# Kernel optimization log

Measured on AMD Instinct MI355X. Metric: run time of the kernel, lower is better.

Reference implementation:

```python
import jax, jax.numpy as jnp
import numpy as np
import math

B_SZ, T, D_IN, D_OUT, N = 8, 4096, 256, 256, 512
RMIN, RMAX, MAX_PHASE = 0.99, 1.0, 6.283


def setup_inputs() -> dict:
    key = jax.random.key(0)
    ks = jax.random.split(key, 8)
    u_in = jax.random.normal(ks[0], (B_SZ, T, D_IN), dtype=jnp.float32)
    u1 = jax.random.uniform(ks[1], (N,), dtype=jnp.float32)
    u2 = jax.random.uniform(ks[2], (N,), dtype=jnp.float32)
    # LRU parametrization from 'Resurrecting Linear Recurrences'
    nu_log = jnp.log(-0.5 * jnp.log(u1 * (RMAX + RMIN) * (RMAX - RMIN) + RMIN ** 2))
    theta_log = jnp.log(MAX_PHASE * u2)
    lambda_mod = jnp.exp(-jnp.exp(nu_log))
    gamma_log = jnp.log(jnp.sqrt(1.0 - jnp.square(lambda_mod)))
    B_real = jax.random.normal(ks[3], (N, D_IN), dtype=jnp.float32) / math.sqrt(2 * D_IN)
    B_imag = jax.random.normal(ks[4], (N, D_IN), dtype=jnp.float32) / math.sqrt(2 * D_IN)
    C_real = jax.random.normal(ks[5], (D_OUT, N), dtype=jnp.float32) / math.sqrt(N)
    C_imag = jax.random.normal(ks[6], (D_OUT, N), dtype=jnp.float32) / math.sqrt(N)
    D = jax.random.normal(ks[7], (D_OUT, D_IN), dtype=jnp.float32) / math.sqrt(D_IN)
    return {"u_in": u_in, "nu_log": nu_log, "theta_log": theta_log,
            "gamma_log": gamma_log, "B_real": B_real, "B_imag": B_imag,
            "C_real": C_real, "C_imag": C_imag, "D": D}


def _lru_forward(u_in, nu_log, theta_log, gamma_log, B_real, B_imag, C_real, C_imag, D):
    lambda_mod = jnp.exp(-jnp.exp(nu_log))
    theta = jnp.exp(theta_log)
    lam = (lambda_mod * jnp.cos(theta) + 1j * lambda_mod * jnp.sin(theta)).astype(jnp.complex64)  # [N]
    gammas = jnp.exp(gamma_log)
    Bc = (B_real + 1j * B_imag).astype(jnp.complex64)  # [N, D_in]
    Cc = (C_real + 1j * C_imag).astype(jnp.complex64)  # [D_out, N]
    # driving term: gamma * (u_t @ B^T)  -> [b, t, n]
    Bu = gammas.astype(jnp.complex64) * jnp.einsum('bti,ni->btn', u_in.astype(jnp.complex64), Bc)
    # linear recurrence x_t = lam * x_{t-1} + Bu_t, x_0 prior = 0, via associative scan
    a = jnp.broadcast_to(lam, Bu.shape)

    def combine(e1, e2):
        a1, b1 = e1
        a2, b2 = e2
        return a1 * a2, a2 * b1 + b2

    _, x = jax.lax.associative_scan(combine, (a, Bu), axis=1)  # [b, t, n] complex
    y = 2.0 * jnp.real(jnp.einsum('btn,on->bto', x, Cc)) + jnp.einsum('bti,oi->bto', u_in, D)
    return y


def reference(u_in, nu_log, theta_log, gamma_log, B_real, B_imag, C_real, C_imag, D):
    return _lru_forward(u_in, nu_log, theta_log, gamma_log, B_real, B_imag, C_real, C_imag, D)
```

## Files before the change

### kernel.cpp

```cpp
#include <hip/hip_runtime.h>
#include <hip/hip_bf16.h>
#include <math.h>

#define B_SZ    8
#define T_LEN   4096
#define DIN     256
#define DOUT    256
#define NST     512
#define M_ROWS  (B_SZ * T_LEN)
#define N1      (2 * NST)
#define K2      (N1 + DIN)
#define CHL     128
#define NCH     (T_LEN / CHL)

typedef __attribute__((ext_vector_type(8))) short bf16x8;
typedef __attribute__((ext_vector_type(4))) float f32x4;
typedef __hip_bfloat16 bf16;

#define OFF_UBF  67108864
#define OFF_WP   83886080
#define OFF_W2   84410368
#define OFF_LAM  85065728
#define OFF_LAML 85069824
#define OFF_SSUM 85073920

__device__ __forceinline__ void gl_lds16(const bf16* g, bf16* l) {
    __builtin_amdgcn_global_load_lds(
        (const __attribute__((address_space(1))) void*)g,
        (__attribute__((address_space(3))) void*)l, 16, 0, 0);
}

__global__ __launch_bounds__(256) void prep(const float* __restrict__ u,
        const float* __restrict__ nu_log, const float* __restrict__ theta_log,
        const float* __restrict__ gamma_log,
        const float* __restrict__ B_real, const float* __restrict__ B_imag,
        const float* __restrict__ C_real, const float* __restrict__ C_imag,
        const float* __restrict__ Dm,
        bf16* __restrict__ ub, bf16* __restrict__ Wp, bf16* __restrict__ W2,
        float* __restrict__ lam, float* __restrict__ lamL) {
    int bid = blockIdx.x, tid = threadIdx.x;
    if (bid < 8192) {
        int i = bid * 256 + tid;
        float4 v = ((const float4*)u)[i];
        union { bf16 h[4]; uint2 u2; } p;
        p.h[0] = __float2bfloat16(v.x); p.h[1] = __float2bfloat16(v.y);
        p.h[2] = __float2bfloat16(v.z); p.h[3] = __float2bfloat16(v.w);
        ((uint2*)ub)[i] = p.u2;
    } else if (bid < 9216) {
        int c = bid - 8192;
        int n = c & (NST - 1);
        float g = expf(gamma_log[n]);
        const float* src = (c < NST) ? (B_real + (size_t)n * DIN)
                                     : (B_imag + (size_t)n * DIN);
        Wp[(size_t)c * DIN + tid] = __float2bfloat16(g * src[tid]);
        int idx = c * 256 + tid;
        if (idx < NST) {
            float lm = expf(-expf(nu_log[idx]));
            float th = expf(theta_log[idx]);
            float lr = lm * cosf(th), li = lm * sinf(th);
            lam[idx] = lr; lam[NST + idx] = li;
            float ar = lr, ai = li;
#pragma unroll
            for (int q = 0; q < 7; ++q) {
                float nr = ar * ar - ai * ai;
                float ni = 2.f * ar * ai;
                ar = nr; ai = ni;
            }
            lamL[idx] = ar; lamL[NST + idx] = ai;
        }
    } else {
        int idx = (bid - 9216) * 256 + tid;
        if (idx < DOUT * K2) {
            int o = idx / K2, c = idx - o * K2;
            float v;
            if (c < NST)            v =  2.0f * C_real[(size_t)o * NST + c];
            else if (c < 2 * NST)   v = -2.0f * C_imag[(size_t)o * NST + (c - NST)];
            else                    v =  Dm[(size_t)o * DIN + (c - 2 * NST)];
            W2[idx] = __float2bfloat16(v);
        }
    }
}

__global__ __launch_bounds__(256) void gemm1(const bf16* __restrict__ u,
                                             const bf16* __restrict__ Wp,
                                             bf16* __restrict__ Bu) {
    __shared__ union {
        bf16 ab[2][2][128 * 32];
        bf16 cs[128 * 136];
    } sm;
    const int tid = threadIdx.x;
    const int m0 = blockIdx.x * 128, n0 = blockIdx.y * 128;
    const int lane = tid & 63, w = tid >> 6;
    const int wm = (w >> 1) * 64, wn = (w & 1) * 64;
    const int lr16 = lane & 15, kq = (lane >> 4) * 8;
    const int srow = tid >> 2, scol = (tid & 3) * 8;

    f32x4 acc[4][4] = {};
    {
        gl_lds16(u  + (size_t)(m0 + srow) * DIN + scol,       &sm.ab[0][0][tid * 8]);
        gl_lds16(u  + (size_t)(m0 + 64 + srow) * DIN + scol,  &sm.ab[0][0][2048 + tid * 8]);
        gl_lds16(Wp + (size_t)(n0 + srow) * DIN + scol,       &sm.ab[0][1][tid * 8]);
        gl_lds16(Wp + (size_t)(n0 + 64 + srow) * DIN + scol,  &sm.ab[0][1][2048 + tid * 8]);
    }
    __syncthreads();
    for (int t = 0; t < 8; ++t) {
        const int cur = t & 1;
        if (t < 7) {
            int k0 = (t + 1) * 32;
            gl_lds16(u  + (size_t)(m0 + srow) * DIN + k0 + scol,       &sm.ab[cur ^ 1][0][tid * 8]);
            gl_lds16(u  + (size_t)(m0 + 64 + srow) * DIN + k0 + scol,  &sm.ab[cur ^ 1][0][2048 + tid * 8]);
            gl_lds16(Wp + (size_t)(n0 + srow) * DIN + k0 + scol,       &sm.ab[cur ^ 1][1][tid * 8]);
            gl_lds16(Wp + (size_t)(n0 + 64 + srow) * DIN + k0 + scol,  &sm.ab[cur ^ 1][1][2048 + tid * 8]);
        }
        bf16x8 af[4], bfr[4];
#pragma unroll
        for (int i = 0; i < 4; ++i)
            af[i] = *(const bf16x8*)(&sm.ab[cur][0][(wm + i * 16 + lr16) * 32 + kq]);
#pragma unroll
        for (int j = 0; j < 4; ++j)
            bfr[j] = *(const bf16x8*)(&sm.ab[cur][1][(wn + j * 16 + lr16) * 32 + kq]);
#pragma unroll
        for (int i = 0; i < 4; ++i)
#pragma unroll
            for (int j = 0; j < 4; ++j)
                acc[i][j] = __builtin_amdgcn_mfma_f32_16x16x32_bf16(af[i], bfr[j], acc[i][j], 0, 0, 0);
        __syncthreads();
    }
    const int crow = (lane >> 4) * 4, ccol = lane & 15;
#pragma unroll
    for (int i = 0; i < 4; ++i)
#pragma unroll
        for (int j = 0; j < 4; ++j)
#pragma unroll
            for (int r = 0; r < 4; ++r)
                sm.cs[(wm + i * 16 + crow + r) * 136 + wn + j * 16 + ccol] =
                    __float2bfloat16(acc[i][j][r]);
    __syncthreads();
#pragma unroll
    for (int p = 0; p < 8; ++p) {
        int row = p * 16 + (tid >> 4);
        int colg = (tid & 15) * 8;
        *(uint4*)(&Bu[(size_t)(m0 + row) * N1 + n0 + colg]) =
            *(const uint4*)(&sm.cs[row * 136 + colg]);
    }
}

__global__ __launch_bounds__(512) void scan1(const bf16* __restrict__ Bu,
                                             const float* __restrict__ lam,
                                             float* __restrict__ Ssum) {
    int n = threadIdx.x;
    int c = blockIdx.x;
    int b = blockIdx.y;
    float lr = lam[n], li = lam[NST + n];
    const bf16* base = Bu + ((size_t)b * T_LEN + (size_t)c * CHL) * N1;
    float sr = 0.f, si = 0.f;
#pragma unroll 8
    for (int j = 0; j < CHL; ++j) {
        float br = __bfloat162float(base[(size_t)j * N1 + n]);
        float bi = __bfloat162float(base[(size_t)j * N1 + NST + n]);
        float tr = lr * sr - li * si + br;
        float ti = lr * si + li * sr + bi;
        sr = tr; si = ti;
    }
    size_t o = ((size_t)b * NCH + c) * N1 + n;
    Ssum[o] = sr; Ssum[o + NST] = si;
}

__global__ __launch_bounds__(512) void scan3(bf16* __restrict__ Bu,
                                             const float* __restrict__ lam,
                                             const float* __restrict__ lamL,
                                             const float* __restrict__ Ssum) {
    int n = threadIdx.x, c = blockIdx.x, b = blockIdx.y;
    float lr = lam[n], li = lam[NST + n];
    float Lr = lamL[n], Li = lamL[NST + n];
    float pr = 0.f, pi = 0.f;
#pragma unroll 4
    for (int cp = 0; cp < c; ++cp) {
        size_t o = ((size_t)b * NCH + cp) * N1 + n;
        float sr = Ssum[o], si = Ssum[o + NST];
        float tr = Lr * pr - Li * pi + sr;
        float ti = Lr * pi + Li * pr + si;
        pr = tr; pi = ti;
    }
    float xr = pr, xi = pi;
    bf16* base = Bu + ((size_t)b * T_LEN + (size_t)c * CHL) * N1;
#pragma unroll 8
    for (int j = 0; j < CHL; ++j) {
        float br = __bfloat162float(base[(size_t)j * N1 + n]);
        float bi = __bfloat162float(base[(size_t)j * N1 + NST + n]);
        float tr = lr * xr - li * xi + br;
        float ti = lr * xi + li * xr + bi;
        xr = tr; xi = ti;
        base[(size_t)j * N1 + n]       = __float2bfloat16(xr);
        base[(size_t)j * N1 + NST + n] = __float2bfloat16(xi);
    }
}

__global__ __launch_bounds__(512) void gemm2(const bf16* __restrict__ X,
                                             const bf16* __restrict__ u,
                                             const bf16* __restrict__ W2,
                                             float* __restrict__ y) {
    __shared__ bf16 ab[2][2][128 * 32];
    const int tid = threadIdx.x;
    const int m0 = blockIdx.x * 128, n0 = blockIdx.y * 128;
    const int lane = tid & 63, w = tid >> 6;
    const int wm = (w >> 2) * 64, wn = (w & 3) * 32;
    const int lr16 = lane & 15, kq = (lane >> 4) * 8;
    const int srow = tid >> 2, scol = (tid & 3) * 8;

    f32x4 acc[4][2] = {};
    gl_lds16(X  + (size_t)(m0 + srow) * N1 + scol,  &ab[0][0][tid * 8]);
    gl_lds16(W2 + (size_t)(n0 + srow) * K2 + scol,  &ab[0][1][tid * 8]);
    __syncthreads();
    for (int t = 0; t < 40; ++t) {
        const int cur = t & 1;
        if (t < 39) {
            int k0 = (t + 1) * 32;
            const bf16* Asrc; size_t lda; int kc;
            if (k0 < N1) { Asrc = X; lda = N1;  kc = k0; }
            else         { Asrc = u; lda = DIN; kc = k0 - N1; }
            gl_lds16(Asrc + (size_t)(m0 + srow) * lda + kc + scol, &ab[cur ^ 1][0][tid * 8]);
            gl_lds16(W2 + (size_t)(n0 + srow) * K2 + k0 + scol,    &ab[cur ^ 1][1][tid * 8]);
        }
        bf16x8 af[4], bfr[2];
#pragma unroll
        for (int i = 0; i < 4; ++i)
            af[i] = *(const bf16x8*)(&ab[cur][0][(wm + i * 16 + lr16) * 32 + kq]);
#pragma unroll
        for (int j = 0; j < 2; ++j)
            bfr[j] = *(const bf16x8*)(&ab[cur][1][(wn + j * 16 + lr16) * 32 + kq]);
#pragma unroll
        for (int i = 0; i < 4; ++i)
#pragma unroll
            for (int j = 0; j < 2; ++j)
                acc[i][j] = __builtin_amdgcn_mfma_f32_16x16x32_bf16(af[i], bfr[j], acc[i][j], 0, 0, 0);
        __syncthreads();
    }
    const int crow = (lane >> 4) * 4, ccol = lane & 15;
#pragma unroll
    for (int i = 0; i < 4; ++i)
#pragma unroll
        for (int j = 0; j < 2; ++j)
#pragma unroll
            for (int r = 0; r < 4; ++r)
                y[(size_t)(m0 + wm + i * 16 + crow + r) * DOUT + n0 + wn + j * 16 + ccol] = acc[i][j][r];
}

extern "C" void kernel_launch(void* const* d_in, const int* in_sizes, int n_in,
                              void* d_out, int out_size, void* d_ws, size_t ws_size,
                              hipStream_t stream) {
    const float* u_in      = (const float*)d_in[0];
    const float* nu_log    = (const float*)d_in[1];
    const float* theta_log = (const float*)d_in[2];
    const float* gamma_log = (const float*)d_in[3];
    const float* B_real    = (const float*)d_in[4];
    const float* B_imag    = (const float*)d_in[5];
    const float* C_real    = (const float*)d_in[6];
    const float* C_imag    = (const float*)d_in[7];
    const float* Dm        = (const float*)d_in[8];
    float* y = (float*)d_out;
    char* ws = (char*)d_ws;

    bf16*  Bu   = (bf16*)ws;
    bf16*  u_bf = (bf16*)(ws + OFF_UBF);
    bf16*  Wp   = (bf16*)(ws + OFF_WP);
    bf16*  W2   = (bf16*)(ws + OFF_W2);
    float* lam  = (float*)(ws + OFF_LAM);
    float* lamL = (float*)(ws + OFF_LAML);
    float* Ssum = (float*)(ws + OFF_SSUM);

    prep<<<10496, 256, 0, stream>>>(u_in, nu_log, theta_log, gamma_log,
                                    B_real, B_imag, C_real, C_imag, Dm,
                                    u_bf, Wp, W2, lam, lamL);
    gemm1<<<dim3(M_ROWS / 128, N1 / 128), 256, 0, stream>>>(u_bf, Wp, Bu);
    scan1<<<dim3(NCH, B_SZ), 512, 0, stream>>>(Bu, lam, Ssum);
    scan3<<<dim3(NCH, B_SZ), 512, 0, stream>>>(Bu, lam, lamL, Ssum);
    gemm2<<<dim3(M_ROWS / 128, DOUT / 128), 512, 0, stream>>>(Bu, u_bf, W2, y);
}
```

Measured before the change: 188.2 us.

## Double gemm2 K-tile to 64 and XOR-swizzle LDS layout to avoid bank conflicts

The output GEMM now stages 64-wide K tiles instead of 32, which halves the loop iterations and barriers. The shared-memory layout uses an XOR swizzle of 16-byte chunks by row, so the MFMA fragment reads avoid LDS bank conflicts. Shared memory per block doubles, which may reduce occupancy. Only gemm2 is affected, and it is one stage of a multi-kernel pipeline.

```diff
diff --git a/kernel.cpp b/kernel.cpp
--- a/kernel.cpp
+++ b/kernel.cpp
@@ -200,42 +200,54 @@
                                              const bf16* __restrict__ u,
                                              const bf16* __restrict__ W2,
                                              float* __restrict__ y) {
-    __shared__ bf16 ab[2][2][128 * 32];
+    __shared__ bf16 ab[2][2][128 * 64];
     const int tid = threadIdx.x;
     const int m0 = blockIdx.x * 128, n0 = blockIdx.y * 128;
     const int lane = tid & 63, w = tid >> 6;
     const int wm = (w >> 2) * 64, wn = (w & 3) * 32;
     const int lr16 = lane & 15, kq = (lane >> 4) * 8;
-    const int srow = tid >> 2, scol = (tid & 3) * 8;
+    const int srow = tid >> 3;
+    const int scolx = ((tid & 7) ^ (srow & 7)) * 8;
+
+#define G2STAGE(buf, t_) do { int k0_ = (t_) * 64;                                    \
+        const bf16* Asrc_; size_t lda_; int kc_;                                      \
+        if (k0_ < N1) { Asrc_ = X; lda_ = N1;  kc_ = k0_; }                           \
+        else          { Asrc_ = u; lda_ = DIN; kc_ = k0_ - N1; }                      \
+        gl_lds16(Asrc_ + (size_t)(m0 + srow) * lda_ + kc_ + scolx,      &ab[buf][0][tid * 8]);        \
+        gl_lds16(Asrc_ + (size_t)(m0 + 64 + srow) * lda_ + kc_ + scolx, &ab[buf][0][4096 + tid * 8]); \
+        gl_lds16(W2 + (size_t)(n0 + srow) * K2 + k0_ + scolx,           &ab[buf][1][tid * 8]);        \
+        gl_lds16(W2 + (size_t)(n0 + 64 + srow) * K2 + k0_ + scolx,      &ab[buf][1][4096 + tid * 8]); \
+    } while (0)
 
     f32x4 acc[4][2] = {};
-    gl_lds16(X  + (size_t)(m0 + srow) * N1 + scol,  &ab[0][0][tid * 8]);
-    gl_lds16(W2 + (size_t)(n0 + srow) * K2 + scol,  &ab[0][1][tid * 8]);
+    G2STAGE(0, 0);
     __syncthreads();
-    for (int t = 0; t < 40; ++t) {
+    for (int t = 0; t < 20; ++t) {
         const int cur = t & 1;
-        if (t < 39) {
-            int k0 = (t + 1) * 32;
-            const bf16* Asrc; size_t lda; int kc;
-            if (k0 < N1) { Asrc = X; lda = N1;  kc = k0; }
-            else         { Asrc = u; lda = DIN; kc = k0 - N1; }
-            gl_lds16(Asrc + (size_t)(m0 + srow) * lda + kc + scol, &ab[cur ^ 1][0][tid * 8]);
-            gl_lds16(W2 + (size_t)(n0 + srow) * K2 + k0 + scol,    &ab[cur ^ 1][1][tid * 8]);
-        }
-        bf16x8 af[4], bfr[2];
-#pragma unroll
-        for (int i = 0; i < 4; ++i)
-            af[i] = *(const bf16x8*)(&ab[cur][0][(wm + i * 16 + lr16) * 32 + kq]);
-#pragma unroll
-        for (int j = 0; j < 2; ++j)
-            bfr[j] = *(const bf16x8*)(&ab[cur][1][(wn + j * 16 + lr16) * 32 + kq]);
-#pragma unroll
-        for (int i = 0; i < 4; ++i)
-#pragma unroll
-            for (int j = 0; j < 2; ++j)
-                acc[i][j] = __builtin_amdgcn_mfma_f32_16x16x32_bf16(af[i], bfr[j], acc[i][j], 0, 0, 0);
+        if (t < 19) G2STAGE(cur ^ 1, t + 1);
+#pragma unroll
+        for (int ks = 0; ks < 2; ++ks) {
+            const int gck = ks * 4 + (lane >> 4);
+            bf16x8 af[4], bfr[2];
+#pragma unroll
+            for (int i = 0; i < 4; ++i) {
+                int row = wm + i * 16 + lr16;
+                af[i] = *(const bf16x8*)(&ab[cur][0][row * 64 + ((gck ^ (lane & 7)) * 8)]);
+            }
+#pragma unroll
+            for (int j = 0; j < 2; ++j) {
+                int row = wn + j * 16 + lr16;
+                bfr[j] = *(const bf16x8*)(&ab[cur][1][row * 64 + ((gck ^ (lane & 7)) * 8)]);
+            }
+#pragma unroll
+            for (int i = 0; i < 4; ++i)
+#pragma unroll
+                for (int j = 0; j < 2; ++j)
+                    acc[i][j] = __builtin_amdgcn_mfma_f32_16x16x32_bf16(af[i], bfr[j], acc[i][j], 0, 0, 0);
+        }
         __syncthreads();
     }
+#undef G2STAGE
     const int crow = (lane >> 4) * 4, ccol = lane & 15;
 #pragma unroll
     for (int i = 0; i < 4; ++i)
```

Result: no change. 184.8 us (-1.8%).
